# Optimization experiments

Hardware: AMD Instinct MI355X
Metric: run time of the kernel (lower is better)

## Reference

```python
import jax, jax.numpy as jnp
import numpy as np

EPS = 1e-5

def _ln(t, g, b):
    m = t.mean(-1, keepdims=True)
    v = ((t - m) ** 2).mean(-1, keepdims=True)
    return (t - m) * jax.lax.rsqrt(v + EPS) * g + b

def _sr(t, w, b, H, W, sr):
    # t: [B, H*W, C] -> spatial-reduction conv -> [B, (H//sr)*(W//sr), C]
    B, L, C = t.shape
    xi = t.transpose(0, 2, 1).reshape(B, C, H, W)
    y = jax.lax.conv_general_dilated(xi, w, (sr, sr), 'VALID',
                                     dimension_numbers=('NCHW', 'OIHW', 'NCHW'))
    return y.reshape(B, C, -1).transpose(0, 2, 1) + b

def setup_inputs() -> dict:
    key = jax.random.key(0)
    ks = jax.random.split(key, 9)
    C, head, sr, H, W = 128, 2, 2, 64, 64
    B, N = 4, 2 * H * W
    s = 0.02
    return {
        'x': jax.random.normal(ks[0], (B, N, C), jnp.float32),
        'qW': jax.random.normal(ks[1], (C, C), jnp.float32) * s,
        'qb': jnp.zeros((C,), jnp.float32),
        'kvW': jax.random.normal(ks[2], (C, 2 * C), jnp.float32) * s,
        'kvb': jnp.zeros((2 * C,), jnp.float32),
        'projW': jax.random.normal(ks[3], (C, C), jnp.float32) * s,
        'projb': jnp.zeros((C,), jnp.float32),
        'srW': jax.random.normal(ks[4], (C, C, sr, sr), jnp.float32) * s,
        'srb': jnp.zeros((C,), jnp.float32),
        'lnW': jnp.ones((C,), jnp.float32),
        'lnB': jnp.zeros((C,), jnp.float32),
        'H': H, 'W': W, 'fuse': 1,
    }

def reference(x, qW, qb, kvW, kvb, projW, projb, srW, srb, lnW, lnB, H, W, fuse):
    head, sr = 2, 2
    B, N, C = x.shape
    Dh = C // head
    scale = Dh ** -0.5
    q = (x @ qW + qb).reshape(B, N, head, Dh).transpose(0, 2, 1, 3)  # [B,h,N,Dh]
    mask = None
    if fuse and sr > 1:
        half = N // 2
        x_rgb = _ln(_sr(x[:, :half, :], srW, srb, H, W, sr), lnW, lnB)
        x_dte = _ln(_sr(x[:, half:, :], srW, srb, H, W, sr), lnW, lnB)
        xkv = jnp.concatenate([x_rgb, x_dte], axis=1)
        M = N // (sr * sr)
        row = jnp.arange(N)[:, None] < half            # query in rgb half
        col = jnp.arange(M)[None, :] < (M // 2)        # key in rgb half
        mask = row == col                              # True on same-modality blocks -> masked
    elif sr > 1:
        xkv = _ln(_sr(x, srW, srb, H, W, sr), lnW, lnB)
    else:
        xkv = x
    M = xkv.shape[1]
    kv = (xkv @ kvW + kvb).reshape(B, M, 2, head, Dh).transpose(2, 0, 3, 1, 4)
    k, v = kv[0], kv[1]                                # [B,h,M,Dh]
    attn = jnp.einsum('bhnd,bhmd->bhnm', q, k) * scale
    if mask is not None:
        attn = jnp.where(mask[None, None], -jnp.inf, attn)
    attn = jax.nn.softmax(attn, axis=-1)
    out = jnp.einsum('bhnm,bhmd->bhnd', attn, v).transpose(0, 2, 1, 3).reshape(B, N, C)
    return out @ projW + projb
```

## Files before the change

### kernel.cpp

```cpp
#include <hip/hip_runtime.h>
#include <hip/hip_bf16.h>

#define LN_EPS 1e-5f

typedef __attribute__((ext_vector_type(8))) short bf16x8_t;
typedef __attribute__((ext_vector_type(4))) short bf16x4_t;
typedef __attribute__((ext_vector_type(4))) float f32x4_t;
typedef __attribute__((ext_vector_type(4))) unsigned short u16x4_t;

#define MFMA32(a, b, c) __builtin_amdgcn_mfma_f32_16x16x32_bf16(a, b, c, 0, 0, 0)
#define MFMA16(a, b, c) __builtin_amdgcn_mfma_f32_16x16x16bf16_1k(a, b, c, 0, 0, 0)

__device__ inline unsigned short f2bf(float f) {
    union { float f; unsigned int u; } v; v.f = f;
    unsigned int r = v.u + 0x7fffu + ((v.u >> 16) & 1u);
    return (unsigned short)(r >> 16);
}

__device__ inline u16x4_t pk4(float a, float b, float c, float d) {
    union { u16x4_t v; __hip_bfloat162 h[2]; } u;
    u.h[0] = __float22bfloat162_rn(float2{a, b});
    u.h[1] = __float22bfloat162_rn(float2{c, d});
    return u.v;
}
__device__ inline bf16x4_t pk4b(float a, float b, float c, float d) {
    union { bf16x4_t v; __hip_bfloat162 h[2]; } u;
    u.h[0] = __float22bfloat162_rn(float2{a, b});
    u.h[1] = __float22bfloat162_rn(float2{c, d});
    return u.v;
}
__device__ inline bf16x8_t pk8(float4 a, float4 b) {
    union { bf16x8_t v; __hip_bfloat162 h[4]; } u;
    u.h[0] = __float22bfloat162_rn(float2{a.x, a.y});
    u.h[1] = __float22bfloat162_rn(float2{a.z, a.w});
    u.h[2] = __float22bfloat162_rn(float2{b.x, b.y});
    u.h[3] = __float22bfloat162_rn(float2{b.z, b.w});
    return u.v;
}

__device__ inline size_t fragidx(int row, int k, int KC) {
    return ((size_t)((row >> 4) * KC + (k >> 5))) * 512 +
           (((k >> 3) & 3) * 16 + (row & 15)) * 8 + (k & 7);
}

__global__ void k_prep_w(const float* __restrict__ qW, const float* __restrict__ kvW,
                         const float* __restrict__ projW, const float* __restrict__ srW,
                         unsigned short* __restrict__ qWs, unsigned short* __restrict__ kvWs,
                         unsigned short* __restrict__ projWs, unsigned short* __restrict__ srWs) {
    int i = blockIdx.x * 256 + threadIdx.x;
    if (i < 16384) {
        int n = i & 127, k = i >> 7;
        qWs[fragidx(n, k, 4)] = f2bf(qW[k * 128 + n]);
    } else if (i < 49152) {
        int j = i - 16384; int n = j & 255, k = j >> 8;
        kvWs[fragidx(n, k, 4)] = f2bf(kvW[k * 256 + n]);
    } else if (i < 65536) {
        int j = i - 49152; int n = j & 127, k = j >> 7;
        projWs[fragidx(n, k, 4)] = f2bf(projW[k * 128 + n]);
    } else {
        int j = i - 65536; int n = j >> 9, rem = j & 511, q = rem >> 7, c = rem & 127;
        srWs[fragidx(n, q * 128 + c, 16)] = f2bf(srW[n * 512 + c * 4 + q]);
    }
}

__global__ void k_prep_x(const float* __restrict__ x, unsigned short* __restrict__ Psw) {
    int i = blockIdx.x * 256 + threadIdx.x;
    int c4 = i & 31;
    int row = i >> 5;
    float4 v = *(const float4*)(x + (size_t)row * 128 + c4 * 4);
    u16x4_t o = pk4(v.x, v.y, v.z, v.w);
    int ch = c4 * 4;
    int b = row >> 13, n = row & 8191;
    int hf = n >> 12, rem = n & 4095;
    int y = rem >> 6, xc = rem & 63;
    int oy = y >> 1, ky = y & 1, ox = xc >> 1, kx = xc & 1;
    int q = ky * 2 + kx;
    int pos = b * 2048 + hf * 1024 + oy * 32 + ox;
    *(u16x4_t*)(Psw + fragidx(pos, q * 128 + ch, 16)) = o;
}

__global__ __launch_bounds__(256)
void k_convkv(const unsigned short* __restrict__ Psw, const unsigned short* __restrict__ srWs,
              const float* __restrict__ srb, const float* __restrict__ lnW,
              const float* __restrict__ lnB, const unsigned short* __restrict__ kvWs,
              const float* __restrict__ kvb, unsigned short* __restrict__ ksw,
              unsigned short* __restrict__ vls) {
    const int t = threadIdx.x, w = t >> 6, lane = t & 63;
    const int col = lane & 15, quad = lane >> 4;
    const int RT = blockIdx.x;

    __shared__ unsigned short xs[4 * 512];
    __shared__ float lnred[4][16][2];

    f32x4_t acc[2] = {};
    {
        const unsigned short* xp = Psw + (size_t)RT * 16 * 512 + lane * 8;
        const unsigned short* wp = srWs + lane * 8;
        for (int kc = 0; kc < 16; kc++) {
            bf16x8_t xb = *(const bf16x8_t*)(xp + (size_t)kc * 512);
            #pragma unroll
            for (int jj = 0; jj < 2; jj++) {
                bf16x8_t wf = *(const bf16x8_t*)(wp + (size_t)((w * 2 + jj) * 16 + kc) * 512);
                acc[jj] = MFMA32(wf, xb, acc[jj]);
            }
        }
    }
    float s = 0.f, ss = 0.f;
    #pragma unroll
    for (int jj = 0; jj < 2; jj++) {
        float4 bs = *(const float4*)(srb + (w * 2 + jj) * 16 + quad * 4);
        acc[jj][0] += bs.x; acc[jj][1] += bs.y; acc[jj][2] += bs.z; acc[jj][3] += bs.w;
        #pragma unroll
        for (int r = 0; r < 4; r++) { float v = acc[jj][r]; s += v; ss += v * v; }
    }
    s += __shfl_xor(s, 16, 64);  s += __shfl_xor(s, 32, 64);
    ss += __shfl_xor(ss, 16, 64); ss += __shfl_xor(ss, 32, 64);
    if (lane < 16) { lnred[w][lane][0] = s; lnred[w][lane][1] = ss; }
    __syncthreads();
    float stot = 0.f, sstot = 0.f;
    #pragma unroll
    for (int ww = 0; ww < 4; ww++) { stot += lnred[ww][col][0]; sstot += lnred[ww][col][1]; }
    float mean = stot * (1.0f / 128.0f);
    float var = sstot * (1.0f / 128.0f) - mean * mean;
    float rs = rsqrtf(var + LN_EPS);
    #pragma unroll
    for (int jj = 0; jj < 2; jj++) {
        int f0 = (w * 2 + jj) * 16 + quad * 4;
        float4 g = *(const float4*)(lnW + f0);
        float4 be = *(const float4*)(lnB + f0);
        u16x4_t o = pk4((acc[jj][0] - mean) * rs * g.x + be.x,
                        (acc[jj][1] - mean) * rs * g.y + be.y,
                        (acc[jj][2] - mean) * rs * g.z + be.z,
                        (acc[jj][3] - mean) * rs * g.w + be.w);
        *(u16x4_t*)(xs + ((size_t)(f0 >> 5)) * 512 +
                    (((f0 >> 3) & 3) * 16 + col) * 8 + (f0 & 7)) = o;
    }
    __syncthreads();
    bf16x8_t xf[4];
    #pragma unroll
    for (int kc = 0; kc < 4; kc++)
        xf[kc] = *(const bf16x8_t*)(xs + (size_t)kc * 512 + lane * 8);
    const int p0 = RT * 16;
    const int bb = p0 >> 11;
    #pragma unroll
    for (int jj = 0; jj < 2; jj++) {
        const int nt = w * 2 + jj;
        f32x4_t aK = {};
        #pragma unroll
        for (int kc = 0; kc < 4; kc++) {
            bf16x8_t wf = *(const bf16x8_t*)(kvWs + (size_t)(nt * 4 + kc) * 512 + lane * 8);
            aK = MFMA32(wf, xf[kc], aK);
        }
        float4 bs = *(const float4*)(kvb + nt * 16 + quad * 4);
        int m = (p0 + col) & 2047;
        int bh = bb * 2 + (nt >> 2);
        int d0 = (nt & 3) * 16 + quad * 4;
        u16x4_t o = pk4(aK[0] + bs.x, aK[1] + bs.y, aK[2] + bs.z, aK[3] + bs.w);
        *(u16x4_t*)(ksw + ((size_t)(bh * 128 + (m >> 4)) * 2 + (d0 >> 5)) * 512 +
                    (((d0 >> 3) & 3) * 16 + (m & 15)) * 8 + (d0 & 7)) = o;
    }
    #pragma unroll
    for (int jj = 0; jj < 2; jj++) {
        const int nt = w * 2 + jj;
        f32x4_t aV = {};
        #pragma unroll
        for (int kc = 0; kc < 4; kc++) {
            bf16x8_t wf = *(const bf16x8_t*)(kvWs + (size_t)((8 + nt) * 4 + kc) * 512 + lane * 8);
            aV = MFMA32(xf[kc], wf, aV);
        }
        int fv = nt * 16 + col;
        int h = fv >> 6, dd = fv & 63;
        float bv = kvb[128 + fv];
        int m0 = (p0 + quad * 4) & 2047;
        int bh = bb * 2 + h;
        int kt = m0 >> 6, nb = (m0 >> 4) & 3;
        u16x4_t o = pk4(aV[0] + bv, aV[1] + bv, aV[2] + bv, aV[3] + bv);
        *(u16x4_t*)(vls + (((size_t)(bh * 32 + kt) * 4 + (dd >> 4)) * 2 + (nb >> 1)) * 512 +
                    (quad * 16 + (dd & 15)) * 8 + (nb & 1) * 4) = o;
    }
}

__global__ __launch_bounds__(256)
void k_attn_f2(const float* __restrict__ x, const unsigned short* __restrict__ qWs,
               const float* __restrict__ qb, const unsigned short* __restrict__ ksw,
               const unsigned short* __restrict__ vls, const unsigned short* __restrict__ projWs,
               const float* __restrict__ projb, float* __restrict__ out) {
    const int blkx = blockIdx.x, mod = blockIdx.y, b = blockIdx.z;
    const int t = threadIdx.x, w = t >> 6, lane = t & 63;
    const int col = lane & 15, quad = lane >> 4;
    const int qg = w & 1, h = w >> 1;
    const int bh = b * 2 + h;
    const int qbase = mod * 4096 + blkx * 64 + qg * 32;

    __shared__ unsigned short sbuf[64 * 136];

    unsigned short* qarea = sbuf + w * 2048;
    const float sc = 0.125f * 1.44269504089f;
    #pragma unroll
    for (int qt = 0; qt < 2; qt++) {
        const float* xrow = x + ((size_t)b * 8192 + qbase + qt * 16 + col) * 128;
        f32x4_t acc[4] = {};
        #pragma unroll
        for (int kc = 0; kc < 4; kc++) {
            float4 xa = *(const float4*)(xrow + kc * 32 + quad * 8);
            float4 xb2 = *(const float4*)(xrow + kc * 32 + quad * 8 + 4);
            bf16x8_t xf = pk8(xa, xb2);
            #pragma unroll
            for (int j = 0; j < 4; j++) {
                bf16x8_t wf = *(const bf16x8_t*)(qWs + (size_t)((h * 4 + j) * 4 + kc) * 512 + lane * 8);
                acc[j] = MFMA32(wf, xf, acc[j]);
            }
        }
        #pragma unroll
        for (int j = 0; j < 4; j++) {
            float4 bs = *(const float4*)(qb + h * 64 + j * 16 + quad * 4);
            u16x4_t o = pk4((acc[j][0] + bs.x) * sc, (acc[j][1] + bs.y) * sc,
                            (acc[j][2] + bs.z) * sc, (acc[j][3] + bs.w) * sc);
            *(u16x4_t*)(qarea + ((size_t)(qt * 2 + (j >> 1))) * 512 +
                        (((j & 1) * 2 + (quad >> 1)) * 16 + col) * 8 + (quad & 1) * 4) = o;
        }
    }
    bf16x8_t qf[2][2];
    #pragma unroll
    for (int qt = 0; qt < 2; qt++)
        #pragma unroll
        for (int kc = 0; kc < 2; kc++)
            qf[qt][kc] = *(const bf16x8_t*)(qarea + (size_t)(qt * 2 + kc) * 512 + lane * 8);
    __syncthreads();

    const unsigned short* kp0 =
        ksw + ((size_t)(bh * 128 + (1 - mod) * 64) * 2) * 512 + lane * 8;
    const unsigned short* vp0 =
        vls + ((size_t)(bh * 32 + (1 - mod) * 16) * 8) * 512 + lane * 8;
    const bf16x4_t ones4 = { 0x3F80, 0x3F80, 0x3F80, 0x3F80 };

    f32x4_t O[2][4] = {};
    f32x4_t accl[2] = {};

    for (int kt = 0; kt < 16; kt++) {
        bf16x8_t kf[8];
        #pragma unroll
        for (int i = 0; i < 8; i++)
            kf[i] = *(const bf16x8_t*)(kp0 + (size_t)(kt * 8 + i) * 512);
        union { bf16x8_t v8; bf16x4_t v4[2]; } vf[8];
        #pragma unroll
        for (int i = 0; i < 8; i++)
            vf[i].v8 = *(const bf16x8_t*)(vp0 + (size_t)(kt * 8 + i) * 512);
        f32x4_t ST[2][4];
        #pragma unroll
        for (int qt = 0; qt < 2; qt++)
            #pragma unroll
            for (int nb = 0; nb < 4; nb++) {
                f32x4_t sA = {};
                sA = MFMA32(kf[nb * 2 + 0], qf[qt][0], sA);
                sA = MFMA32(kf[nb * 2 + 1], qf[qt][1], sA);
                ST[qt][nb] = sA;
            }
        bf16x4_t pa[2][4];
        #pragma unroll
        for (int qt = 0; qt < 2; qt++)
            #pragma unroll
            for (int nb = 0; nb < 4; nb++)
                pa[qt][nb] = pk4b(exp2f(ST[qt][nb][0]), exp2f(ST[qt][nb][1]),
                                  exp2f(ST[qt][nb][2]), exp2f(ST[qt][nb][3]));
        #pragma unroll
        for (int qt = 0; qt < 2; qt++) {
            #pragma unroll
            for (int nb = 0; nb < 4; nb++) {
                accl[qt] = MFMA16(pa[qt][nb], ones4, accl[qt]);
                #pragma unroll
                for (int dt = 0; dt < 4; dt++)
                    O[qt][dt] = MFMA16(pa[qt][nb], vf[dt * 2 + (nb >> 1)].v4[nb & 1], O[qt][dt]);
            }
        }
    }

    #pragma unroll
    for (int qt = 0; qt < 2; qt++) {
        #pragma unroll
        for (int r = 0; r < 4; r++) {
            float rl = 1.0f / accl[qt][r];
            int qrow = qg * 32 + qt * 16 + quad * 4 + r;
            #pragma unroll
            for (int dt = 0; dt < 4; dt++)
                sbuf[qrow * 136 + h * 64 + dt * 16 + col] = f2bf(O[qt][dt][r] * rl);
        }
    }
    __syncthreads();
    {
        const int qt2 = w;
        bf16x8_t ob[4];
        #pragma unroll
        for (int kc = 0; kc < 4; kc++)
            ob[kc] = *(const bf16x8_t*)(sbuf + (size_t)(qt2 * 16 + col) * 136 + kc * 32 + quad * 8);
        f32x4_t acc[8];
        #pragma unroll
        for (int j = 0; j < 8; j++) acc[j] = f32x4_t{};
        #pragma unroll
        for (int kc = 0; kc < 4; kc++)
            #pragma unroll
            for (int j = 0; j < 8; j++) {
                bf16x8_t wf = *(const bf16x8_t*)(projWs + (size_t)(j * 4 + kc) * 512 + lane * 8);
                acc[j] = MFMA32(wf, ob[kc], acc[j]);
            }
        const int n = b * 8192 + mod * 4096 + blkx * 64 + qt2 * 16 + col;
        #pragma unroll
        for (int j = 0; j < 8; j++) {
            int f0 = j * 16 + quad * 4;
            float4 bs = *(const float4*)(projb + f0);
            float4 o = { acc[j][0] + bs.x, acc[j][1] + bs.y,
                         acc[j][2] + bs.z, acc[j][3] + bs.w };
            *(float4*)(out + (size_t)n * 128 + f0) = o;
        }
    }
}

extern "C" void kernel_launch(void* const* d_in, const int* in_sizes, int n_in,
                              void* d_out, int out_size, void* d_ws, size_t ws_size,
                              hipStream_t stream) {
    const float* x     = (const float*)d_in[0];
    const float* qW    = (const float*)d_in[1];
    const float* qb    = (const float*)d_in[2];
    const float* kvW   = (const float*)d_in[3];
    const float* kvb   = (const float*)d_in[4];
    const float* projW = (const float*)d_in[5];
    const float* projb = (const float*)d_in[6];
    const float* srW   = (const float*)d_in[7];
    const float* srb   = (const float*)d_in[8];
    const float* lnW   = (const float*)d_in[9];
    const float* lnB   = (const float*)d_in[10];

    char* ws = (char*)d_ws;
    unsigned short* qWs    = (unsigned short*)(ws + 0);
    unsigned short* kvWs   = (unsigned short*)(ws + 32768);
    unsigned short* projWs = (unsigned short*)(ws + 98304);
    unsigned short* srWs   = (unsigned short*)(ws + 131072);
    unsigned short* Psw    = (unsigned short*)(ws + 262144);
    unsigned short* ksw    = (unsigned short*)(ws + 8650752);
    unsigned short* vls    = (unsigned short*)(ws + 10747904);

    k_prep_w<<<dim3(512), dim3(256), 0, stream>>>(qW, kvW, projW, srW,
                                                  qWs, kvWs, projWs, srWs);
    k_prep_x<<<dim3(4096), dim3(256), 0, stream>>>(x, Psw);
    k_convkv<<<dim3(512), dim3(256), 0, stream>>>(Psw, srWs, srb, lnW, lnB,
                                                  kvWs, kvb, ksw, vls);
    k_attn_f2<<<dim3(64, 2, 4), dim3(256), 0, stream>>>(x, qWs, qb, ksw, vls,
                                                        projWs, projb, (float*)d_out);
}
```

Before: 146.8 us.

## Fuse input patch gather into conv kernel and split attention keys across waves

```diff
diff --git a/kernel.cpp b/kernel.cpp
--- a/kernel.cpp
+++ b/kernel.cpp
@@ -63,24 +63,8 @@
     }
 }
 
-__global__ void k_prep_x(const float* __restrict__ x, unsigned short* __restrict__ Psw) {
-    int i = blockIdx.x * 256 + threadIdx.x;
-    int c4 = i & 31;
-    int row = i >> 5;
-    float4 v = *(const float4*)(x + (size_t)row * 128 + c4 * 4);
-    u16x4_t o = pk4(v.x, v.y, v.z, v.w);
-    int ch = c4 * 4;
-    int b = row >> 13, n = row & 8191;
-    int hf = n >> 12, rem = n & 4095;
-    int y = rem >> 6, xc = rem & 63;
-    int oy = y >> 1, ky = y & 1, ox = xc >> 1, kx = xc & 1;
-    int q = ky * 2 + kx;
-    int pos = b * 2048 + hf * 1024 + oy * 32 + ox;
-    *(u16x4_t*)(Psw + fragidx(pos, q * 128 + ch, 16)) = o;
-}
-
 __global__ __launch_bounds__(256)
-void k_convkv(const unsigned short* __restrict__ Psw, const unsigned short* __restrict__ srWs,
+void k_convkv(const float* __restrict__ x, const unsigned short* __restrict__ srWs,
               const float* __restrict__ srb, const float* __restrict__ lnW,
               const float* __restrict__ lnB, const unsigned short* __restrict__ kvWs,
               const float* __restrict__ kvb, unsigned short* __restrict__ ksw,
@@ -92,12 +76,26 @@
     __shared__ unsigned short xs[4 * 512];
     __shared__ float lnred[4][16][2];
 
+    const int pos = RT * 16 + col;
+    const int pb = pos >> 11, phf = (pos >> 10) & 1;
+    const int poy = (pos >> 5) & 31, pox = pos & 31;
+    int rowbase[4];
+    #pragma unroll
+    for (int q = 0; q < 4; q++) {
+        int ky = q >> 1, kx = q & 1;
+        int n = phf * 4096 + (2 * poy + ky) * 64 + 2 * pox + kx;
+        rowbase[q] = (pb * 8192 + n) * 128;
+    }
+
     f32x4_t acc[2] = {};
     {
-        const unsigned short* xp = Psw + (size_t)RT * 16 * 512 + lane * 8;
         const unsigned short* wp = srWs + lane * 8;
+        #pragma unroll
         for (int kc = 0; kc < 16; kc++) {
-            bf16x8_t xb = *(const bf16x8_t*)(xp + (size_t)kc * 512);
+            const float* xr = x + rowbase[kc >> 2] + (kc & 3) * 32 + quad * 8;
+            float4 xa = *(const float4*)(xr);
+            float4 xb2 = *(const float4*)(xr + 4);
+            bf16x8_t xb = pk8(xa, xb2);
             #pragma unroll
             for (int jj = 0; jj < 2; jj++) {
                 bf16x8_t wf = *(const bf16x8_t*)(wp + (size_t)((w * 2 + jj) * 16 + kc) * 512);
@@ -181,24 +179,26 @@
 }
 
 __global__ __launch_bounds__(256)
-void k_attn_f2(const float* __restrict__ x, const unsigned short* __restrict__ qWs,
+void k_attn_f3(const float* __restrict__ x, const unsigned short* __restrict__ qWs,
                const float* __restrict__ qb, const unsigned short* __restrict__ ksw,
                const unsigned short* __restrict__ vls, const unsigned short* __restrict__ projWs,
                const float* __restrict__ projb, float* __restrict__ out) {
     const int blkx = blockIdx.x, mod = blockIdx.y, b = blockIdx.z;
     const int t = threadIdx.x, w = t >> 6, lane = t & 63;
     const int col = lane & 15, quad = lane >> 4;
-    const int qg = w & 1, h = w >> 1;
+    const int h = w & 1, ks = w >> 1;
     const int bh = b * 2 + h;
-    const int qbase = mod * 4096 + blkx * 64 + qg * 32;
-
-    __shared__ unsigned short sbuf[64 * 136];
-
-    unsigned short* qarea = sbuf + w * 2048;
-    const float sc = 0.125f * 1.44269504089f;
-    #pragma unroll
-    for (int qt = 0; qt < 2; qt++) {
+    const int qbase = mod * 4096 + blkx * 32;
+
+    __shared__ float Ocomb[2 * 32 * 64];
+    __shared__ float lcomb[64];
+    __shared__ unsigned short rows[32 * 136];
+    __shared__ unsigned short qfr[2 * 4 * 512];
+
+    {
+        const int qt = ks;
         const float* xrow = x + ((size_t)b * 8192 + qbase + qt * 16 + col) * 128;
+        const float sc = 0.125f * 1.44269504089f;
         f32x4_t acc[4] = {};
         #pragma unroll
         for (int kc = 0; kc < 4; kc++) {
@@ -216,17 +216,18 @@
             float4 bs = *(const float4*)(qb + h * 64 + j * 16 + quad * 4);
             u16x4_t o = pk4((acc[j][0] + bs.x) * sc, (acc[j][1] + bs.y) * sc,
                             (acc[j][2] + bs.z) * sc, (acc[j][3] + bs.w) * sc);
-            *(u16x4_t*)(qarea + ((size_t)(qt * 2 + (j >> 1))) * 512 +
+            *(u16x4_t*)(qfr + (size_t)h * 2048 + ((size_t)(qt * 2 + (j >> 1))) * 512 +
                         (((j & 1) * 2 + (quad >> 1)) * 16 + col) * 8 + (quad & 1) * 4) = o;
         }
     }
+    __syncthreads();
     bf16x8_t qf[2][2];
     #pragma unroll
     for (int qt = 0; qt < 2; qt++)
         #pragma unroll
         for (int kc = 0; kc < 2; kc++)
-            qf[qt][kc] = *(const bf16x8_t*)(qarea + (size_t)(qt * 2 + kc) * 512 + lane * 8);
-    __syncthreads();
+            qf[qt][kc] = *(const bf16x8_t*)(qfr + (size_t)h * 2048 +
+                                            (size_t)(qt * 2 + kc) * 512 + lane * 8);
 
     const unsigned short* kp0 =
         ksw + ((size_t)(bh * 128 + (1 - mod) * 64) * 2) * 512 + lane * 8;
@@ -237,7 +238,7 @@
     f32x4_t O[2][4] = {};
     f32x4_t accl[2] = {};
 
-    for (int kt = 0; kt < 16; kt++) {
+    for (int kt = ks * 8; kt < ks * 8 + 8; kt++) {
         bf16x8_t kf[8];
         #pragma unroll
         for (int i = 0; i < 8; i++)
@@ -275,24 +276,41 @@
         }
     }
 
-    #pragma unroll
-    for (int qt = 0; qt < 2; qt++) {
-        #pragma unroll
-        for (int r = 0; r < 4; r++) {
-            float rl = 1.0f / accl[qt][r];
-            int qrow = qg * 32 + qt * 16 + quad * 4 + r;
-            #pragma unroll
-            for (int dt = 0; dt < 4; dt++)
-                sbuf[qrow * 136 + h * 64 + dt * 16 + col] = f2bf(O[qt][dt][r] * rl);
-        }
-    }
-    __syncthreads();
-    {
-        const int qt2 = w;
+    if (ks == 1) {
+        #pragma unroll
+        for (int qt = 0; qt < 2; qt++)
+            #pragma unroll
+            for (int r = 0; r < 4; r++) {
+                int qrow = qt * 16 + quad * 4 + r;
+                #pragma unroll
+                for (int dt = 0; dt < 4; dt++)
+                    Ocomb[(h * 32 + qrow) * 64 + dt * 16 + col] = O[qt][dt][r];
+                if (col == 0) lcomb[h * 32 + qrow] = accl[qt][r];
+            }
+    }
+    __syncthreads();
+    if (ks == 0) {
+        #pragma unroll
+        for (int qt = 0; qt < 2; qt++)
+            #pragma unroll
+            for (int r = 0; r < 4; r++) {
+                int qrow = qt * 16 + quad * 4 + r;
+                float lt = accl[qt][r] + lcomb[h * 32 + qrow];
+                float rl = 1.0f / lt;
+                #pragma unroll
+                for (int dt = 0; dt < 4; dt++) {
+                    float ov = O[qt][dt][r] + Ocomb[(h * 32 + qrow) * 64 + dt * 16 + col];
+                    rows[qrow * 136 + h * 64 + dt * 16 + col] = f2bf(ov * rl);
+                }
+            }
+    }
+    __syncthreads();
+    if (ks == 0) {
+        const int qt2 = h;
         bf16x8_t ob[4];
         #pragma unroll
         for (int kc = 0; kc < 4; kc++)
-            ob[kc] = *(const bf16x8_t*)(sbuf + (size_t)(qt2 * 16 + col) * 136 + kc * 32 + quad * 8);
+            ob[kc] = *(const bf16x8_t*)(rows + (size_t)(qt2 * 16 + col) * 136 + kc * 32 + quad * 8);
         f32x4_t acc[8];
         #pragma unroll
         for (int j = 0; j < 8; j++) acc[j] = f32x4_t{};
@@ -303,7 +321,7 @@
                 bf16x8_t wf = *(const bf16x8_t*)(projWs + (size_t)(j * 4 + kc) * 512 + lane * 8);
                 acc[j] = MFMA32(wf, ob[kc], acc[j]);
             }
-        const int n = b * 8192 + mod * 4096 + blkx * 64 + qt2 * 16 + col;
+        const int n = b * 8192 + qbase + qt2 * 16 + col;
         #pragma unroll
         for (int j = 0; j < 8; j++) {
             int f0 = j * 16 + quad * 4;
@@ -335,15 +353,13 @@
     unsigned short* kvWs   = (unsigned short*)(ws + 32768);
     unsigned short* projWs = (unsigned short*)(ws + 98304);
     unsigned short* srWs   = (unsigned short*)(ws + 131072);
-    unsigned short* Psw    = (unsigned short*)(ws + 262144);
-    unsigned short* ksw    = (unsigned short*)(ws + 8650752);
-    unsigned short* vls    = (unsigned short*)(ws + 10747904);
+    unsigned short* ksw    = (unsigned short*)(ws + 262144);
+    unsigned short* vls    = (unsigned short*)(ws + 2359296);
 
     k_prep_w<<<dim3(512), dim3(256), 0, stream>>>(qW, kvW, projW, srW,
                                                   qWs, kvWs, projWs, srWs);
-    k_prep_x<<<dim3(4096), dim3(256), 0, stream>>>(x, Psw);
-    k_convkv<<<dim3(512), dim3(256), 0, stream>>>(Psw, srWs, srb, lnW, lnB,
+    k_convkv<<<dim3(512), dim3(256), 0, stream>>>(x, srWs, srb, lnW, lnB,
                                                   kvWs, kvb, ksw, vls);
-    k_attn_f2<<<dim3(64, 2, 4), dim3(256), 0, stream>>>(x, qWs, qb, ksw, vls,
-                                                        projWs, projb, (float*)d_out);
-}
+    k_attn_f3<<<dim3(128, 2, 4), dim3(256), 0, stream>>>(x, qWs, qb, ksw, vls,
+                                                         projWs, projb, (float*)d_out);
+}
```

Result: no change. 149.5 us (+1.8%).

## Fuse x im2col/bf16 conversion into conv-KV kernel and use hardware exp2

Applied to the files above, without the earlier changes.

```diff
diff --git a/kernel.cpp b/kernel.cpp
--- a/kernel.cpp
+++ b/kernel.cpp
@@ -10,6 +10,16 @@
 
 #define MFMA32(a, b, c) __builtin_amdgcn_mfma_f32_16x16x32_bf16(a, b, c, 0, 0, 0)
 #define MFMA16(a, b, c) __builtin_amdgcn_mfma_f32_16x16x16bf16_1k(a, b, c, 0, 0, 0)
+
+__device__ inline float fast_exp2(float x) {
+#if __has_builtin(__builtin_amdgcn_exp2f)
+    return __builtin_amdgcn_exp2f(x);
+#else
+    float r;
+    asm volatile("v_exp_f32 %0, %1\n\ts_nop 0" : "=v"(r) : "v"(x));
+    return r;
+#endif
+}
 
 __device__ inline unsigned short f2bf(float f) {
     union { float f; unsigned int u; } v; v.f = f;
@@ -63,24 +73,8 @@
     }
 }
 
-__global__ void k_prep_x(const float* __restrict__ x, unsigned short* __restrict__ Psw) {
-    int i = blockIdx.x * 256 + threadIdx.x;
-    int c4 = i & 31;
-    int row = i >> 5;
-    float4 v = *(const float4*)(x + (size_t)row * 128 + c4 * 4);
-    u16x4_t o = pk4(v.x, v.y, v.z, v.w);
-    int ch = c4 * 4;
-    int b = row >> 13, n = row & 8191;
-    int hf = n >> 12, rem = n & 4095;
-    int y = rem >> 6, xc = rem & 63;
-    int oy = y >> 1, ky = y & 1, ox = xc >> 1, kx = xc & 1;
-    int q = ky * 2 + kx;
-    int pos = b * 2048 + hf * 1024 + oy * 32 + ox;
-    *(u16x4_t*)(Psw + fragidx(pos, q * 128 + ch, 16)) = o;
-}
-
 __global__ __launch_bounds__(256)
-void k_convkv(const unsigned short* __restrict__ Psw, const unsigned short* __restrict__ srWs,
+void k_convkv(const float* __restrict__ x, const unsigned short* __restrict__ srWs,
               const float* __restrict__ srb, const float* __restrict__ lnW,
               const float* __restrict__ lnB, const unsigned short* __restrict__ kvWs,
               const float* __restrict__ kvb, unsigned short* __restrict__ ksw,
@@ -92,12 +86,26 @@
     __shared__ unsigned short xs[4 * 512];
     __shared__ float lnred[4][16][2];
 
+    const int pos = RT * 16 + col;
+    const int pb = pos >> 11, phf = (pos >> 10) & 1;
+    const int poy = (pos >> 5) & 31, pox = pos & 31;
+    int rowbase[4];
+    #pragma unroll
+    for (int q = 0; q < 4; q++) {
+        int ky = q >> 1, kx = q & 1;
+        int n = phf * 4096 + (2 * poy + ky) * 64 + 2 * pox + kx;
+        rowbase[q] = (pb * 8192 + n) * 128;
+    }
+
     f32x4_t acc[2] = {};
     {
-        const unsigned short* xp = Psw + (size_t)RT * 16 * 512 + lane * 8;
         const unsigned short* wp = srWs + lane * 8;
+        #pragma unroll
         for (int kc = 0; kc < 16; kc++) {
-            bf16x8_t xb = *(const bf16x8_t*)(xp + (size_t)kc * 512);
+            const float* xr = x + rowbase[kc >> 2] + (kc & 3) * 32 + quad * 8;
+            float4 xa = *(const float4*)(xr);
+            float4 xb2 = *(const float4*)(xr + 4);
+            bf16x8_t xb = pk8(xa, xb2);
             #pragma unroll
             for (int jj = 0; jj < 2; jj++) {
                 bf16x8_t wf = *(const bf16x8_t*)(wp + (size_t)((w * 2 + jj) * 16 + kc) * 512);
@@ -181,7 +189,7 @@
 }
 
 __global__ __launch_bounds__(256)
-void k_attn_f2(const float* __restrict__ x, const unsigned short* __restrict__ qWs,
+void k_attn_f5(const float* __restrict__ x, const unsigned short* __restrict__ qWs,
                const float* __restrict__ qb, const unsigned short* __restrict__ ksw,
                const unsigned short* __restrict__ vls, const unsigned short* __restrict__ projWs,
                const float* __restrict__ projb, float* __restrict__ out) {
@@ -261,8 +269,8 @@
         for (int qt = 0; qt < 2; qt++)
             #pragma unroll
             for (int nb = 0; nb < 4; nb++)
-                pa[qt][nb] = pk4b(exp2f(ST[qt][nb][0]), exp2f(ST[qt][nb][1]),
-                                  exp2f(ST[qt][nb][2]), exp2f(ST[qt][nb][3]));
+                pa[qt][nb] = pk4b(fast_exp2(ST[qt][nb][0]), fast_exp2(ST[qt][nb][1]),
+                                  fast_exp2(ST[qt][nb][2]), fast_exp2(ST[qt][nb][3]));
         #pragma unroll
         for (int qt = 0; qt < 2; qt++) {
             #pragma unroll
@@ -335,15 +343,13 @@
     unsigned short* kvWs   = (unsigned short*)(ws + 32768);
     unsigned short* projWs = (unsigned short*)(ws + 98304);
     unsigned short* srWs   = (unsigned short*)(ws + 131072);
-    unsigned short* Psw    = (unsigned short*)(ws + 262144);
-    unsigned short* ksw    = (unsigned short*)(ws + 8650752);
-    unsigned short* vls    = (unsigned short*)(ws + 10747904);
+    unsigned short* ksw    = (unsigned short*)(ws + 262144);
+    unsigned short* vls    = (unsigned short*)(ws + 2359296);
 
     k_prep_w<<<dim3(512), dim3(256), 0, stream>>>(qW, kvW, projW, srW,
                                                   qWs, kvWs, projWs, srWs);
-    k_prep_x<<<dim3(4096), dim3(256), 0, stream>>>(x, Psw);
-    k_convkv<<<dim3(512), dim3(256), 0, stream>>>(Psw, srWs, srb, lnW, lnB,
+    k_convkv<<<dim3(512), dim3(256), 0, stream>>>(x, srWs, srb, lnW, lnB,
                                                   kvWs, kvb, ksw, vls);
-    k_attn_f2<<<dim3(64, 2, 4), dim3(256), 0, stream>>>(x, qWs, qb, ksw, vls,
+    k_attn_f5<<<dim3(64, 2, 4), dim3(256), 0, stream>>>(x, qWs, qb, ksw, vls,
                                                         projWs, projb, (float*)d_out);
 }
```

New measurement: 136.9 us. 6.8% less time.
